# Kernel optimization log

Measured on AMD Instinct MI355X. Metric: run time of the kernel, lower is better.

The kernel has to match this reference:

```python
import jax, jax.numpy as jnp
import numpy as np

QMAX = 127.0  # 2**(8-1) - 1 for n_bits=8

def fake_quant_last_dim(t):
    # per-row absmax fake quant over last dim (per-token for acts, per-channel for weights)
    scales = jnp.max(jnp.abs(t), axis=-1, keepdims=True)
    scales = jnp.clip(scales, 1e-05, None) / QMAX
    return jnp.round(t / scales) * scales

def setup_inputs() -> dict:
    key = jax.random.key(0)
    k1, k2, k3 = jax.random.split(key, 3)
    B, S, D_in, D_out = 4, 2048, 4096, 4096
    return {
        "input": jax.random.normal(k1, (B, S, D_in), dtype=jnp.float32),
        "weight": jax.random.normal(k2, (D_out, D_in), dtype=jnp.float32) * 0.02,
        "bias": jax.random.normal(k3, (D_out,), dtype=jnp.float32) * 0.02,
    }

def reference(input, weight, bias):
    w_q = fake_quant_last_dim(weight)          # per-output-channel
    x_q = fake_quant_last_dim(input)           # per-token
    y = jnp.einsum('bsi,oi->bso', x_q, w_q) + bias
    return fake_quant_last_dim(y)              # per-token output quant
```

## Files before the change

kernel.cpp:

```cpp
#include <hip/hip_runtime.h>

typedef unsigned int u32;
typedef __attribute__((ext_vector_type(4))) int i32x4;

#define BM 256
#define BN 256
#define BKT 64

__device__ __forceinline__ void gload16(const void* g, void* l) {
  __builtin_amdgcn_global_load_lds(
      (const __attribute__((address_space(1))) unsigned int*)g,
      (__attribute__((address_space(3))) unsigned int*)l, 16, 0, 0);
}

__device__ __forceinline__ u32 pack4_i8(float4 v, float scale) {
  const int a = (int)rintf(v.x / scale);
  const int b = (int)rintf(v.y / scale);
  const int c = (int)rintf(v.z / scale);
  const int d = (int)rintf(v.w / scale);
  return (u32)(a & 255) | (((u32)(b & 255)) << 8) |
         (((u32)(c & 255)) << 16) | (((u32)(d & 255)) << 24);
}

__global__ __launch_bounds__(256) void quant_rows4096_dual_kernel(
    const float* __restrict__ xsrc, const float* __restrict__ wsrc,
    u32* __restrict__ qx, u32* __restrict__ qw,
    float* __restrict__ sx, float* __restrict__ sw, int mrows)
{
  const int bid = (int)blockIdx.x;
  const float* __restrict__ src;
  u32* __restrict__ q;
  float* __restrict__ scales;
  size_t row;
  if (bid < mrows) { src = xsrc; q = qx; scales = sx; row = (size_t)bid; }
  else             { src = wsrc; q = qw; scales = sw; row = (size_t)(bid - mrows); }

  const float4* __restrict__ p = (const float4*)(src + row * 4096);
  const int t = threadIdx.x;
  float4 v0 = p[t];
  float4 v1 = p[t + 256];
  float4 v2 = p[t + 512];
  float4 v3 = p[t + 768];
  float m = 0.0f;
  m = fmaxf(m, fmaxf(fmaxf(fabsf(v0.x), fabsf(v0.y)), fmaxf(fabsf(v0.z), fabsf(v0.w))));
  m = fmaxf(m, fmaxf(fmaxf(fabsf(v1.x), fabsf(v1.y)), fmaxf(fabsf(v1.z), fabsf(v1.w))));
  m = fmaxf(m, fmaxf(fmaxf(fabsf(v2.x), fabsf(v2.y)), fmaxf(fabsf(v2.z), fabsf(v2.w))));
  m = fmaxf(m, fmaxf(fmaxf(fabsf(v3.x), fabsf(v3.y)), fmaxf(fabsf(v3.z), fabsf(v3.w))));
  #pragma unroll
  for (int off = 32; off > 0; off >>= 1) m = fmaxf(m, __shfl_xor(m, off));
  __shared__ float wmax[4];
  if ((t & 63) == 0) wmax[t >> 6] = m;
  __syncthreads();
  m = fmaxf(fmaxf(wmax[0], wmax[1]), fmaxf(wmax[2], wmax[3]));
  const float scale = fmaxf(m, 1e-5f) * (1.0f / 127.0f);
  if (t == 0) scales[row] = scale;
  u32* __restrict__ qp = q + row * 1024;
  qp[t]       = pack4_i8(v0, scale);
  qp[t + 256] = pack4_i8(v1, scale);
  qp[t + 512] = pack4_i8(v2, scale);
  qp[t + 768] = pack4_i8(v3, scale);
}

__global__ __launch_bounds__(256) void quant_rows_kernel(
    const float* __restrict__ src, u32* __restrict__ q,
    float* __restrict__ scales, int K)
{
  const size_t row = blockIdx.x;
  const float* __restrict__ p = src + row * (size_t)K;
  const int t = threadIdx.x;
  const int nv = K >> 2;
  float m = 0.0f;
  for (int i = t; i < nv; i += 256) {
    float4 v = ((const float4*)p)[i];
    m = fmaxf(m, fmaxf(fmaxf(fabsf(v.x), fabsf(v.y)),
                       fmaxf(fabsf(v.z), fabsf(v.w))));
  }
  #pragma unroll
  for (int off = 32; off > 0; off >>= 1) m = fmaxf(m, __shfl_xor(m, off));
  __shared__ float wmax[4];
  if ((t & 63) == 0) wmax[t >> 6] = m;
  __syncthreads();
  m = fmaxf(fmaxf(wmax[0], wmax[1]), fmaxf(wmax[2], wmax[3]));
  const float scale = fmaxf(m, 1e-5f) * (1.0f / 127.0f);
  if (t == 0) scales[row] = scale;
  u32* __restrict__ qp = q + row * ((size_t)K >> 2);
  for (int i = t; i < nv; i += 256) {
    float4 v = ((const float4*)p)[i];
    qp[i] = pack4_i8(v, scale);
  }
}

__global__ __launch_bounds__(512, 2) void gemm_bt_kernel(
    const signed char* __restrict__ Aq, const signed char* __restrict__ Bq,
    const float* __restrict__ sx, const float* __restrict__ sw,
    const float* __restrict__ bias, float* __restrict__ Y,
    unsigned int* __restrict__ rowmax, int M, int N, int K)
{
  __shared__ signed char lds[4][2][BM * 64];

  int bid = (int)blockIdx.x;
  const int nwg = (int)gridDim.x;
  if ((nwg & 7) == 0) {
    const int cpx = nwg >> 3;
    bid = (bid & 7) * cpx + (bid >> 3);
  }
  const int ntile = N / BN;
  const size_t brow = (size_t)(bid / ntile) * BM;
  const size_t bcol = (size_t)(bid % ntile) * BN;

  const int t = threadIdx.x;
  const int lane = t & 63;
  const int wid = t >> 6;
  const int wr = wid >> 2, wc = wid & 3;
  const int g4 = lane >> 4, l16 = lane & 15;

  const int parity = l16 & 1;
  const int w8 = (l16 >> 1) & 7;
  const int sp = (g4 + (parity << 2)) ^ w8;
  const int abase = (wr * 64 + (l16 >> 1)) * 128 + sp * 16;
  const int bbase = (wc * 32 + (l16 >> 1)) * 128 + sp * 16;

  const int q0 = (t & 7) ^ ((t >> 3) & 7);
  const int srow = 2 * (t >> 3) + (q0 >> 2);
  const int scol = (q0 & 3) * 16;
  const signed char* srcA = Aq + (brow + srow) * (size_t)K + scol;
  const signed char* srcB = Bq + (bcol + srow) * (size_t)K + scol;
  const int dstb = t * 16;

  i32x4 acc0[4][4] = {};
  i32x4 acc1[4][4] = {};
  const int nK = K / BKT;

  i32x4 aA0, aA1, aA2, aA3;
  i32x4 aC0, aC1, aC2, aC3;
  i32x4 bA0, bA1, bA2, bA3;

#define STAGE4(S, TT) do { \
    gload16(srcA + (size_t)(TT) * 64,                      &lds[S][0][dstb]); \
    gload16(srcA + 128 * (size_t)K + (size_t)(TT) * 64,    &lds[S][0][8192 + dstb]); \
    gload16(srcB + (size_t)(TT) * 64,                      &lds[S][1][dstb]); \
    gload16(srcB + 128 * (size_t)K + (size_t)(TT) * 64,    &lds[S][1][8192 + dstb]); \
  } while (0)
#define BARS() do { asm volatile("" ::: "memory"); \
                    __builtin_amdgcn_s_barrier(); \
                    asm volatile("" ::: "memory"); } while (0)
#define VMWS(NN) asm volatile("s_waitcnt vmcnt(" #NN ")" ::: "memory")
#define RDA(P, S, MH) do { \
    P##0 = *(const i32x4*)&lds[S][0][abase + (MH) * 4096 +    0]; \
    P##1 = *(const i32x4*)&lds[S][0][abase + (MH) * 4096 + 1024]; \
    P##2 = *(const i32x4*)&lds[S][0][abase + (MH) * 4096 + 2048]; \
    P##3 = *(const i32x4*)&lds[S][0][abase + (MH) * 4096 + 3072]; } while (0)
#define RDB(P, S) do { \
    P##0 = *(const i32x4*)&lds[S][1][bbase +    0]; \
    P##1 = *(const i32x4*)&lds[S][1][bbase + 1024]; \
    P##2 = *(const i32x4*)&lds[S][1][bbase + 2048]; \
    P##3 = *(const i32x4*)&lds[S][1][bbase + 3072]; } while (0)
#define MF(ACC, A, B) do { \
    ACC[0][0] = __builtin_amdgcn_mfma_i32_16x16x64_i8(A##0, B##0, ACC[0][0], 0, 0, 0); \
    ACC[0][1] = __builtin_amdgcn_mfma_i32_16x16x64_i8(A##0, B##1, ACC[0][1], 0, 0, 0); \
    ACC[0][2] = __builtin_amdgcn_mfma_i32_16x16x64_i8(A##0, B##2, ACC[0][2], 0, 0, 0); \
    ACC[0][3] = __builtin_amdgcn_mfma_i32_16x16x64_i8(A##0, B##3, ACC[0][3], 0, 0, 0); \
    ACC[1][0] = __builtin_amdgcn_mfma_i32_16x16x64_i8(A##1, B##0, ACC[1][0], 0, 0, 0); \
    ACC[1][1] = __builtin_amdgcn_mfma_i32_16x16x64_i8(A##1, B##1, ACC[1][1], 0, 0, 0); \
    ACC[1][2] = __builtin_amdgcn_mfma_i32_16x16x64_i8(A##1, B##2, ACC[1][2], 0, 0, 0); \
    ACC[1][3] = __builtin_amdgcn_mfma_i32_16x16x64_i8(A##1, B##3, ACC[1][3], 0, 0, 0); \
    ACC[2][0] = __builtin_amdgcn_mfma_i32_16x16x64_i8(A##2, B##0, ACC[2][0], 0, 0, 0); \
    ACC[2][1] = __builtin_amdgcn_mfma_i32_16x16x64_i8(A##2, B##1, ACC[2][1], 0, 0, 0); \
    ACC[2][2] = __builtin_amdgcn_mfma_i32_16x16x64_i8(A##2, B##2, ACC[2][2], 0, 0, 0); \
    ACC[2][3] = __builtin_amdgcn_mfma_i32_16x16x64_i8(A##2, B##3, ACC[2][3], 0, 0, 0); \
    ACC[3][0] = __builtin_amdgcn_mfma_i32_16x16x64_i8(A##3, B##0, ACC[3][0], 0, 0, 0); \
    ACC[3][1] = __builtin_amdgcn_mfma_i32_16x16x64_i8(A##3, B##1, ACC[3][1], 0, 0, 0); \
    ACC[3][2] = __builtin_amdgcn_mfma_i32_16x16x64_i8(A##3, B##2, ACC[3][2], 0, 0, 0); \
    ACC[3][3] = __builtin_amdgcn_mfma_i32_16x16x64_i8(A##3, B##3, ACC[3][3], 0, 0, 0); } while (0)

#define WIN(S, ST, TT, HASVM, VN) do { \
    if (ST) STAGE4((S + 3) & 3, TT); \
    RDA(aA, S, 0); \
    RDB(bA, S); \
    RDA(aC, S, 1); \
    if (HASVM) { VMWS(VN); } \
    BARS(); \
    __builtin_amdgcn_s_setprio(1); \
    MF(acc0, aA, bA); \
    MF(acc1, aC, bA); \
    __builtin_amdgcn_s_setprio(0); \
  } while (0)

  STAGE4(0, 0);
  STAGE4(1, 1);
  STAGE4(2, 2);
  VMWS(8);
  BARS();

  int kt = 0;
  for (; kt + 8 <= nK; kt += 4) {
    WIN(0, 1, kt + 3, 1, 8);
    WIN(1, 1, kt + 4, 1, 8);
    WIN(2, 1, kt + 5, 1, 8);
    WIN(3, 1, kt + 6, 1, 8);
  }
  WIN(0, 1, nK - 1, 1, 8);
  WIN(1, 0, 0, 1, 4);
  WIN(2, 0, 0, 1, 0);
  WIN(3, 0, 0, 0, 0);

  float swv[4], biv[4];
  size_t gcolv[4];
  #pragma unroll
  for (int j = 0; j < 4; ++j) {
    gcolv[j] = bcol + wc * 64 + j * 16 + l16;
    swv[j] = sw[gcolv[j]];
    biv[j] = bias[gcolv[j]];
  }
  #pragma unroll
  for (int mh = 0; mh < 2; ++mh) {
    #pragma unroll
    for (int i = 0; i < 4; ++i) {
      #pragma unroll
      for (int r = 0; r < 4; ++r) {
        const size_t grow = brow + (size_t)(wr * 128 + mh * 64 + i * 16 + g4 * 4 + r);
        const float sxr = sx[grow];
        float* yrow = Y + grow * (size_t)N;
        float rmax = 0.0f;
        #pragma unroll
        for (int j = 0; j < 4; ++j) {
          const int av = mh ? acc1[i][j][r] : acc0[i][j][r];
          const float y = (float)av * (sxr * swv[j]) + biv[j];
          yrow[gcolv[j]] = y;
          rmax = fmaxf(rmax, fabsf(y));
        }
        rmax = fmaxf(rmax, __shfl_xor(rmax, 1));
        rmax = fmaxf(rmax, __shfl_xor(rmax, 2));
        rmax = fmaxf(rmax, __shfl_xor(rmax, 4));
        rmax = fmaxf(rmax, __shfl_xor(rmax, 8));
        if (l16 == 0)
          atomicMax(&rowmax[grow], __float_as_uint(rmax));
      }
    }
  }
#undef STAGE4
#undef BARS
#undef VMWS
#undef RDA
#undef RDB
#undef MF
#undef WIN
}

__global__ __launch_bounds__(256) void outquant_kernel(
    float* __restrict__ Y, const unsigned int* __restrict__ rowmax, int N)
{
  const size_t row = blockIdx.x;
  const float amax = __uint_as_float(rowmax[row]);
  const float scale = fmaxf(amax, 1e-5f) * (1.0f / 127.0f);
  float* __restrict__ p = Y + row * (size_t)N;
  const int nv = N >> 2;
  for (int i = threadIdx.x; i < nv; i += 256) {
    float4 v = ((float4*)p)[i];
    v.x = rintf(v.x / scale) * scale;
    v.y = rintf(v.y / scale) * scale;
    v.z = rintf(v.z / scale) * scale;
    v.w = rintf(v.w / scale) * scale;
    ((float4*)p)[i] = v;
  }
}

extern "C" void kernel_launch(void* const* d_in, const int* in_sizes, int n_in,
                              void* d_out, int out_size, void* d_ws, size_t ws_size,
                              hipStream_t stream)
{
  const float* x = (const float*)d_in[0];
  const float* wgt = (const float*)d_in[1];
  const float* bias = (const float*)d_in[2];
  float* out = (float*)d_out;

  const int N = in_sizes[2];
  const int K = in_sizes[1] / N;
  const int M = in_sizes[0] / K;

  char* ws = (char*)d_ws;
  signed char* qx = (signed char*)ws;  ws += (size_t)M * K;
  signed char* qw = (signed char*)ws;  ws += (size_t)N * K;
  float* sx = (float*)ws;              ws += (size_t)M * sizeof(float);
  float* sw = (float*)ws;              ws += (size_t)N * sizeof(float);
  unsigned int* rowmax = (unsigned int*)ws;

  hipMemsetAsync(rowmax, 0, (size_t)M * sizeof(unsigned int), stream);

  if (K == 4096) {
    quant_rows4096_dual_kernel<<<M + N, 256, 0, stream>>>(
        x, wgt, (u32*)qx, (u32*)qw, sx, sw, M);
  } else {
    quant_rows_kernel<<<M, 256, 0, stream>>>(x, (u32*)qx, sx, K);
    quant_rows_kernel<<<N, 256, 0, stream>>>(wgt, (u32*)qw, sw, K);
  }

  const int grid = (M / BM) * (N / BN);
  gemm_bt_kernel<<<grid, 512, 0, stream>>>(qx, qw, sx, sw, bias, out, rowmax, M, N, K);

  outquant_kernel<<<M, 256, 0, stream>>>(out, rowmax, N);
}
```

Before: 246.0 us.

## Double-buffer MFMA operand registers to prefetch next LDS stage mid-window

Splits the A/B fragment registers into even and odd sets. Each window now reads the next stage's fragments from LDS between its two MFMA groups, instead of reading the current stage before the barrier. The aim is to hide LDS read latency behind matrix-core work and shorten the critical path around the barrier. The cost is roughly doubled operand register use, which could hurt occupancy or cause spills.

```diff
diff --git a/kernel.cpp b/kernel.cpp
--- a/kernel.cpp
+++ b/kernel.cpp
@@ -131,9 +131,8 @@
   i32x4 acc1[4][4] = {};
   const int nK = K / BKT;
 
-  i32x4 aA0, aA1, aA2, aA3;
-  i32x4 aC0, aC1, aC2, aC3;
-  i32x4 bA0, bA1, bA2, bA3;
+  i32x4 aAe0, aAe1, aAe2, aAe3, aCe0, aCe1, aCe2, aCe3, bAe0, bAe1, bAe2, bAe3;
+  i32x4 aAo0, aAo1, aAo2, aAo3, aCo0, aCo1, aCo2, aCo3, bAo0, bAo1, bAo2, bAo3;
 
 #define STAGE4(S, TT) do { \
     gload16(srcA + (size_t)(TT) * 64,                      &lds[S][0][dstb]); \
@@ -155,6 +154,8 @@
     P##1 = *(const i32x4*)&lds[S][1][bbase + 1024]; \
     P##2 = *(const i32x4*)&lds[S][1][bbase + 2048]; \
     P##3 = *(const i32x4*)&lds[S][1][bbase + 3072]; } while (0)
+#define READF(SET, S) do { \
+    RDA(aA##SET, S, 0); RDB(bA##SET, S); RDA(aC##SET, S, 1); } while (0)
 #define MF(ACC, A, B) do { \
     ACC[0][0] = __builtin_amdgcn_mfma_i32_16x16x64_i8(A##0, B##0, ACC[0][0], 0, 0, 0); \
     ACC[0][1] = __builtin_amdgcn_mfma_i32_16x16x64_i8(A##0, B##1, ACC[0][1], 0, 0, 0); \
@@ -173,16 +174,16 @@
     ACC[3][2] = __builtin_amdgcn_mfma_i32_16x16x64_i8(A##3, B##2, ACC[3][2], 0, 0, 0); \
     ACC[3][3] = __builtin_amdgcn_mfma_i32_16x16x64_i8(A##3, B##3, ACC[3][3], 0, 0, 0); } while (0)
 
-#define WIN(S, ST, TT, HASVM, VN) do { \
+#define WIN(S, CUR, NXT, ST, TT, HASVM, VN, RD) do { \
     if (ST) STAGE4((S + 3) & 3, TT); \
-    RDA(aA, S, 0); \
-    RDB(bA, S); \
-    RDA(aC, S, 1); \
     if (HASVM) { VMWS(VN); } \
     BARS(); \
     __builtin_amdgcn_s_setprio(1); \
-    MF(acc0, aA, bA); \
-    MF(acc1, aC, bA); \
+    MF(acc0, aA##CUR, bA##CUR); \
+    __builtin_amdgcn_s_setprio(0); \
+    if (RD) READF(NXT, (S + 1) & 3); \
+    __builtin_amdgcn_s_setprio(1); \
+    MF(acc1, aC##CUR, bA##CUR); \
     __builtin_amdgcn_s_setprio(0); \
   } while (0)
 
@@ -191,18 +192,19 @@
   STAGE4(2, 2);
   VMWS(8);
   BARS();
+  READF(e, 0);
 
   int kt = 0;
   for (; kt + 8 <= nK; kt += 4) {
-    WIN(0, 1, kt + 3, 1, 8);
-    WIN(1, 1, kt + 4, 1, 8);
-    WIN(2, 1, kt + 5, 1, 8);
-    WIN(3, 1, kt + 6, 1, 8);
-  }
-  WIN(0, 1, nK - 1, 1, 8);
-  WIN(1, 0, 0, 1, 4);
-  WIN(2, 0, 0, 1, 0);
-  WIN(3, 0, 0, 0, 0);
+    WIN(0, e, o, 1, kt + 3, 1, 8, 1);
+    WIN(1, o, e, 1, kt + 4, 1, 8, 1);
+    WIN(2, e, o, 1, kt + 5, 1, 8, 1);
+    WIN(3, o, e, 1, kt + 6, 1, 8, 1);
+  }
+  WIN(0, e, o, 1, nK - 1, 1, 8, 1);
+  WIN(1, o, e, 0, 0, 1, 4, 1);
+  WIN(2, e, o, 0, 0, 1, 0, 1);
+  WIN(3, o, e, 0, 0, 0, 0, 0);
 
   float swv[4], biv[4];
   size_t gcolv[4];
@@ -243,6 +245,7 @@
 #undef VMWS
 #undef RDA
 #undef RDB
+#undef READF
 #undef MF
 #undef WIN
 }
```

Result: slower. 288.0 us (+17.0%).
